# Optimization experiments

Measured on AMD Instinct MI355X. Metric: run time of the kernel, lower is better.

## Reference

```python
import jax, jax.numpy as jnp
import numpy as np

C, H = 256, 8
D = C // H
L, T, R = 2, 2, 3
OUT = 64
N = (30000, 50000)          # (author, paper)
F_IN = (128, 256)
E = (300000, 300000, 400000)
ETYPES = ((0, 1, 0), (1, 0, 1), (1, 1, 2))  # (src_type, dst_type, rel_idx)
SCALE = 1.0 / float(np.sqrt(D))


def setup_inputs() -> dict:
    key = jax.random.key(0)
    ks = iter(jax.random.split(key, 40))
    def nrm(shape, scale):
        return jax.random.normal(next(ks), shape, dtype=jnp.float32) * scale
    inp = {
        "x_author": nrm((N[0], F_IN[0]), 1.0),
        "x_paper": nrm((N[1], F_IN[1]), 1.0),
        "lin_in_author_W": nrm((F_IN[0], C), F_IN[0] ** -0.5),
        "lin_in_author_b": jnp.zeros((C,), jnp.float32),
        "lin_in_paper_W": nrm((F_IN[1], C), F_IN[1] ** -0.5),
        "lin_in_paper_b": jnp.zeros((C,), jnp.float32),
        "k_W": nrm((L, T, C, C), C ** -0.5), "k_b": jnp.zeros((L, T, C), jnp.float32),
        "q_W": nrm((L, T, C, C), C ** -0.5), "q_b": jnp.zeros((L, T, C), jnp.float32),
        "v_W": nrm((L, T, C, C), C ** -0.5), "v_b": jnp.zeros((L, T, C), jnp.float32),
        "a_W": nrm((L, R, H, D, D), D ** -0.5),
        "m_W": nrm((L, R, H, D, D), D ** -0.5),
        "p_rel": jnp.ones((L, R, H), jnp.float32),
        "skip": jnp.ones((L, T), jnp.float32),
        "out_W": nrm((L, T, C, C), C ** -0.5), "out_b": jnp.zeros((L, T, C), jnp.float32),
        "lin_out_W": nrm((C, OUT), C ** -0.5), "lin_out_b": jnp.zeros((OUT,), jnp.float32),
    }
    names = ("ei_writes", "ei_rev_writes", "ei_cites")
    for name, (s, d, _), e in zip(names, ETYPES, E):
        src = jax.random.randint(next(ks), (e,), 0, N[s], dtype=jnp.int32)
        dst = jax.random.randint(next(ks), (e,), 0, N[d], dtype=jnp.int32)
        inp[name] = jnp.stack([src, dst])
    inp["targetnode"] = 0
    return inp


def _seg_softmax(logits, seg, num_segments):
    # numerically stable softmax over ragged groups of edges sharing a dst node
    m = jax.ops.segment_max(logits, seg, num_segments=num_segments)
    m = jnp.where(jnp.isfinite(m), m, 0.0)
    ex = jnp.exp(logits - m[seg])
    s = jax.ops.segment_sum(ex, seg, num_segments=num_segments)
    return ex / (s[seg] + 1e-16)


def _hgt_forward(x_author, x_paper,
                 lin_in_author_W, lin_in_author_b, lin_in_paper_W, lin_in_paper_b,
                 k_W, k_b, q_W, q_b, v_W, v_b, a_W, m_W, p_rel, skip,
                 out_W, out_b, lin_out_W, lin_out_b, eis):
    # per-type input projection + relu
    xs = [
        jax.nn.relu(x_author @ lin_in_author_W + lin_in_author_b),
        jax.nn.relu(x_paper @ lin_in_paper_W + lin_in_paper_b),
    ]
    for l in range(L):
        # per node type k/q/v: [N_t, H, D]
        k = [(xs[t] @ k_W[l, t] + k_b[l, t]).reshape(N[t], H, D) for t in range(T)]
        q = [(xs[t] @ q_W[l, t] + q_b[l, t]).reshape(N[t], H, D) for t in range(T)]
        v = [(xs[t] @ v_W[l, t] + v_b[l, t]).reshape(N[t], H, D) for t in range(T)]
        agg = [jnp.zeros((N[t], H, D), xs[t].dtype) for t in range(T)]
        for (s, d, r), ei in zip(ETYPES, eis):
            src, dst = ei[0], ei[1]
            # relation-specific head-wise transforms of source keys/values
            k_r = jnp.einsum('nhd,hde->nhe', k[s], a_W[l, r])
            v_r = jnp.einsum('nhd,hde->nhe', v[s], m_W[l, r])
            # per-edge attention logits [E, H]
            alpha = jnp.einsum('ehd,ehd->eh', q[d][dst], k_r[src]) * p_rel[l, r] * SCALE
            w = _seg_softmax(alpha, dst, N[d])
            agg[d] = agg[d] + jax.ops.segment_sum(v_r[src] * w[..., None], dst,
                                                  num_segments=N[d])
        new_xs = []
        for t in range(T):
            o = jax.nn.gelu(agg[t].reshape(N[t], C)) @ out_W[l, t] + out_b[l, t]
            beta = jax.nn.sigmoid(skip[l, t])
            new_xs.append(beta * o + (1.0 - beta) * xs[t])
        xs = new_xs
    # shared output linear per node type
    return tuple(x @ lin_out_W + lin_out_b for x in xs)


def reference(x_author, x_paper, lin_in_author_W, lin_in_author_b,
              lin_in_paper_W, lin_in_paper_b, k_W, k_b, q_W, q_b, v_W, v_b,
              a_W, m_W, p_rel, skip, out_W, out_b, lin_out_W, lin_out_b,
              ei_writes, ei_rev_writes, ei_cites, targetnode):
    eis = (ei_writes, ei_rev_writes, ei_cites)
    return _hgt_forward(x_author, x_paper,
                        lin_in_author_W, lin_in_author_b,
                        lin_in_paper_W, lin_in_paper_b,
                        k_W, k_b, q_W, q_b, v_W, v_b, a_W, m_W, p_rel, skip,
                        out_W, out_b, lin_out_W, lin_out_b, eis)
```

## Files before the change

### kernel.cpp

```cpp
#include <hip/hip_runtime.h>


#define CC 256
#define HH 8
#define DD 32
#define LL 2
#define TT 2
#define RR 3
#define OUTD 64

typedef unsigned short bf16_t;
struct us4 { unsigned short x, y, z, w; };
typedef __attribute__((ext_vector_type(8))) short short8;
typedef __attribute__((ext_vector_type(4))) float f32x4;

__device__ __forceinline__ float b2f(unsigned short u) {
  return __uint_as_float(((unsigned)u) << 16);
}
__device__ __forceinline__ float blo(unsigned u) {
  return __uint_as_float(u << 16);
}
__device__ __forceinline__ float bhi(unsigned u) {
  return __uint_as_float(u & 0xFFFF0000u);
}
__device__ __forceinline__ unsigned short f2b(float f) {
  unsigned u = __float_as_uint(f);
  unsigned r = (u + 0x7FFFu + ((u >> 16) & 1u)) >> 16;
  return (unsigned short)r;
}
__device__ __forceinline__ float ld_dyn(const void* p, size_t e, bool isb) {
  return isb ? b2f(((const bf16_t*)p)[e]) : ((const float*)p)[e];
}
__device__ __forceinline__ float4 load4_dyn(const void* p, size_t e, bool isb) {
  if (isb) {
    us4 v = *(const us4*)((const bf16_t*)p + e);
    return make_float4(b2f(v.x), b2f(v.y), b2f(v.z), b2f(v.w));
  }
  return *(const float4*)((const float*)p + e);
}
__device__ __forceinline__ void st_dyn(void* p, size_t e, float v, bool isb) {
  if (isb) ((bf16_t*)p)[e] = f2b(v);
  else ((float*)p)[e] = v;
}
__device__ __forceinline__ float gelu1(float v) {
  const float t = tanhf(0.7978845608028654f * (v + 0.044715f * v * v * v));
  return 0.5f * v * (1.f + t);
}

__global__ void detect_kernel(const unsigned* __restrict__ probe,
                              int* __restrict__ flag) {
  *flag = (*probe == 0x3F800000u) ? 0 : 1;
}

__global__ __launch_bounds__(256) void prep_kernel(
    const void* __restrict__ xA, const void* __restrict__ xP,
    const void* __restrict__ WinA, const void* __restrict__ WinP,
    const void* __restrict__ qW, const void* __restrict__ outW,
    const void* __restrict__ binA, const void* __restrict__ binP,
    const void* __restrict__ qb, const void* __restrict__ ob,
    bf16_t* __restrict__ dq0, bf16_t* __restrict__ dq1,
    bf16_t* __restrict__ dWinAt, bf16_t* __restrict__ dWinPt,
    bf16_t* __restrict__ dqWt, bf16_t* __restrict__ doutWt,
    float* __restrict__ dbinA, float* __restrict__ dbinP,
    float* __restrict__ dqb, float* __restrict__ dob,
    int* __restrict__ zbase, int zn, int N0, int N1,
    const int* __restrict__ dflag) {
  const bool isb = (*dflag != 0);
  int gid = blockIdx.x * 256 + threadIdx.x;
  const int n0 = N0 * 128, n1 = N1 * 256;
  if (gid < n0) { dq0[gid] = f2b(ld_dyn(xA, gid, isb)); return; }
  gid -= n0;
  if (gid < n1) { dq1[gid] = f2b(ld_dyn(xP, gid, isb)); return; }
  gid -= n1;
  if (gid < 128 * 256) {
    const int n = gid % 256, k = gid / 256;
    dWinAt[n * 128 + k] = f2b(ld_dyn(WinA, gid, isb));
    return;
  }
  gid -= 128 * 256;
  if (gid < 256 * 256) {
    const int n = gid % 256, k = gid / 256;
    dWinPt[n * 256 + k] = f2b(ld_dyn(WinP, gid, isb));
    return;
  }
  gid -= 256 * 256;
  if (gid < 4 * 65536) {
    const int lt = gid >> 16, i = gid & 65535;
    const int n = i % 256, k = i / 256;
    dqWt[(size_t)lt * 65536 + n * 256 + k] =
        f2b(ld_dyn(qW, (size_t)lt * 65536 + i, isb));
    return;
  }
  gid -= 4 * 65536;
  if (gid < 4 * 65536) {
    const int lt = gid >> 16, i = gid & 65535;
    const int n = i % 256, k = i / 256;
    doutWt[(size_t)lt * 65536 + n * 256 + k] =
        f2b(ld_dyn(outW, (size_t)lt * 65536 + i, isb));
    return;
  }
  gid -= 4 * 65536;
  if (gid < 256) { dbinA[gid] = ld_dyn(binA, gid, isb); return; }
  gid -= 256;
  if (gid < 256) { dbinP[gid] = ld_dyn(binP, gid, isb); return; }
  gid -= 256;
  if (gid < 1024) { dqb[gid] = ld_dyn(qb, gid, isb); return; }
  gid -= 1024;
  if (gid < 1024) { dob[gid] = ld_dyn(ob, gid, isb); return; }
  gid -= 1024;
  if (gid < zn) zbase[gid] = 0;
}

__global__ __launch_bounds__(256) void fuse_w_kernel(
    const void* __restrict__ kW, const void* __restrict__ vW,
    const void* __restrict__ kb, const void* __restrict__ vb,
    const void* __restrict__ aW, const void* __restrict__ mW,
    bf16_t* __restrict__ Wcat, float* __restrict__ bcat,
    const int* __restrict__ dflag) {
  const bool isb = (*dflag != 0);
  const int lr = blockIdx.x;
  const int l = lr / RR;
  const int r = lr % RR;
  const int which = blockIdx.y;
  const int h = blockIdx.z;
  const int srct[RR] = {0, 1, 1};
  const int s = srct[r];
  __shared__ float Amat[DD][DD];
  const void* Ap = (which == 0 ? aW : mW);
  const size_t Apoff = (size_t)(lr * HH + h) * DD * DD;
  for (int i = threadIdx.x; i < DD * DD; i += 256)
    Amat[i / DD][i % DD] = ld_dyn(Ap, Apoff + i, isb);
  __syncthreads();
  const void* Wsrc = (which == 0 ? kW : vW);
  const void* bsrc = (which == 0 ? kb : vb);
  const size_t Wsoff = (size_t)(l * TT + s) * CC * CC;
  const size_t bsoff = (size_t)(l * TT + s) * CC;
  bf16_t* Wt = Wcat + (size_t)lr * 512 * CC;
  float* bdst = bcat + (size_t)lr * 512;
  const int c = threadIdx.x;
  float wrow[DD];
#pragma unroll
  for (int d = 0; d < DD; ++d)
    wrow[d] = ld_dyn(Wsrc, Wsoff + (size_t)c * CC + h * DD + d, isb);
#pragma unroll 4
  for (int e = 0; e < DD; ++e) {
    float acc = 0.f;
#pragma unroll
    for (int d = 0; d < DD; ++d) acc += wrow[d] * Amat[d][e];
    const int clo = h * DD + e;
    const int phys = ((clo >> 2) << 3) + (which << 2) + (clo & 3);
    Wt[(size_t)phys * CC + c] = f2b(acc);
  }
  if (c < DD) {
    float acc = 0.f;
#pragma unroll
    for (int d = 0; d < DD; ++d)
      acc += ld_dyn(bsrc, bsoff + h * DD + d, isb) * Amat[d][c];
    const int clo = h * DD + c;
    const int phys = ((clo >> 2) << 3) + (which << 2) + (clo & 3);
    bdst[phys] = acc;
  }
}

struct GSeg {
  const bf16_t* A;
  const bf16_t* Bt;
  const float* bias;
  const bf16_t* Sold;
  bf16_t* C;
  int M, N, K, epi, skipIdx, nbx, blk0;
};
struct GBatch {
  GSeg s[6];
  int nseg;
};

__global__ __launch_bounds__(256) void bgemm_kernel(
    GBatch gb, const void* __restrict__ skipv, const int* __restrict__ dflag) {
  __shared__ bf16_t Asb[128][72];
  __shared__ bf16_t Bsb[128][72];
  int si = 0;
#pragma unroll
  for (int t = 1; t < 6; ++t)
    if (t < gb.nseg && (int)blockIdx.x >= gb.s[t].blk0) si = t;
  const bf16_t* __restrict__ A = gb.s[si].A;
  const bf16_t* __restrict__ Bt = gb.s[si].Bt;
  const float* __restrict__ bias = gb.s[si].bias;
  const bf16_t* __restrict__ Sold = gb.s[si].Sold;
  bf16_t* __restrict__ Cm = gb.s[si].C;
  const int M = gb.s[si].M;
  const int N = gb.s[si].N;
  const int K = gb.s[si].K;
  const int epi = gb.s[si].epi;
  const int local = (int)blockIdx.x - gb.s[si].blk0;
  const int bn = (local % gb.s[si].nbx) * 128;
  const int bm = (local / gb.s[si].nbx) * 128;
  const int tid = threadIdx.x;
  const int wave = tid >> 6;
  const int lane = tid & 63;
  const int qd = lane >> 4;
  const int l16 = lane & 15;
  const int wm = (wave & 1) * 64;
  const int wn = (wave >> 1) * 64;
  f32x4 acc[4][4] = {};
  for (int k0 = 0; k0 < K; k0 += 64) {
#pragma unroll
    for (int i = 0; i < 4; ++i) {
      const int c = tid + 256 * i;
      const int row = c >> 3;
      const int col = (c & 7) * 8;
      uint4 va = make_uint4(0u, 0u, 0u, 0u);
      if (bm + row < M)
        va = *(const uint4*)(A + (size_t)(bm + row) * K + k0 + col);
      *(uint4*)&Asb[row][col] = va;
      const uint4 vb = *(const uint4*)(Bt + (size_t)(bn + row) * K + k0 + col);
      *(uint4*)&Bsb[row][col] = vb;
    }
    __syncthreads();
#pragma unroll
    for (int s = 0; s < 2; ++s) {
      short8 af[4], bf[4];
#pragma unroll
      for (int i = 0; i < 4; ++i) {
        af[i] = *(const short8*)&Asb[wm + i * 16 + l16][s * 32 + qd * 8];
        bf[i] = *(const short8*)&Bsb[wn + i * 16 + l16][s * 32 + qd * 8];
      }
#pragma unroll
      for (int mi = 0; mi < 4; ++mi)
#pragma unroll
        for (int ni = 0; ni < 4; ++ni)
          acc[mi][ni] = __builtin_amdgcn_mfma_f32_16x16x32_bf16(
              af[mi], bf[ni], acc[mi][ni], 0, 0, 0);
    }
    __syncthreads();
  }
  float beta = 0.f;
  if (epi == 2)
    beta = 1.f / (1.f + __expf(-ld_dyn(skipv, gb.s[si].skipIdx, *dflag != 0)));
#pragma unroll
  for (int mi = 0; mi < 4; ++mi) {
#pragma unroll
    for (int r = 0; r < 4; ++r) {
      const int row = bm + wm + mi * 16 + qd * 4 + r;
      if (row < M) {
#pragma unroll
        for (int ni = 0; ni < 4; ++ni) {
          const int col = bn + wn + ni * 16 + l16;
          float v = acc[mi][ni][r] + bias[col];
          if (epi == 1) v = fmaxf(v, 0.f);
          if (epi == 2)
            v = beta * v + (1.f - beta) * b2f(Sold[(size_t)row * N + col]);
          Cm[(size_t)row * N + col] = f2b(v);
        }
      }
    }
  }
}

__global__ __launch_bounds__(256) void fgemm2_kernel(
    const bf16_t* __restrict__ A0, int M0, const bf16_t* __restrict__ A1,
    int M1, const void* __restrict__ B, const void* __restrict__ bias,
    void* __restrict__ Cm, const int* __restrict__ dflag) {
  const bool isb = (*dflag != 0);
  __shared__ float As[32][68];
  __shared__ float Bs[32][64];
  const int nb0 = (M0 + 63) / 64;
  const bf16_t* A;
  int M, bm;
  size_t Coff;
  if ((int)blockIdx.x < nb0) {
    A = A0; M = M0; Coff = 0; bm = blockIdx.x * 64;
  } else {
    A = A1; M = M1; Coff = (size_t)M0 * OUTD; bm = (blockIdx.x - nb0) * 64;
  }
  const int tid = threadIdx.x;
  const int tx = tid & 15;
  const int ty = tid >> 4;
  float acc[4][4] = {};
  for (int k0 = 0; k0 < CC; k0 += 32) {
    {
      const int r = tid >> 3;
      const int c4 = (tid & 7) << 2;
#pragma unroll
      for (int rr = 0; rr < 2; ++rr) {
        const int row = bm + r + rr * 32;
        float4 v = make_float4(0.f, 0.f, 0.f, 0.f);
        if (row < M) v = load4_dyn(A, (size_t)row * CC + k0 + c4, true);
        As[c4 + 0][r + rr * 32] = v.x;
        As[c4 + 1][r + rr * 32] = v.y;
        As[c4 + 2][r + rr * 32] = v.z;
        As[c4 + 3][r + rr * 32] = v.w;
      }
    }
    {
      const int r = tid >> 4;
      const int c4 = (tid & 15) << 2;
#pragma unroll
      for (int rr = 0; rr < 2; ++rr) {
        const float4 v =
            load4_dyn(B, (size_t)(k0 + r + rr * 16) * OUTD + c4, isb);
        *(float4*)&Bs[r + rr * 16][c4] = v;
      }
    }
    __syncthreads();
#pragma unroll
    for (int kk = 0; kk < 32; ++kk) {
      const float4 av = *(const float4*)&As[kk][ty << 2];
      const float4 bv = *(const float4*)&Bs[kk][tx << 2];
      acc[0][0] += av.x * bv.x; acc[0][1] += av.x * bv.y;
      acc[0][2] += av.x * bv.z; acc[0][3] += av.x * bv.w;
      acc[1][0] += av.y * bv.x; acc[1][1] += av.y * bv.y;
      acc[1][2] += av.y * bv.z; acc[1][3] += av.y * bv.w;
      acc[2][0] += av.z * bv.x; acc[2][1] += av.z * bv.y;
      acc[2][2] += av.z * bv.z; acc[2][3] += av.z * bv.w;
      acc[3][0] += av.w * bv.x; acc[3][1] += av.w * bv.y;
      acc[3][2] += av.w * bv.z; acc[3][3] += av.w * bv.w;
    }
    __syncthreads();
  }
#pragma unroll
  for (int i = 0; i < 4; ++i) {
    const int row = bm + (ty << 2) + i;
    if (row < M) {
#pragma unroll
      for (int j = 0; j < 4; ++j) {
        const int col = (tx << 2) + j;
        const float v = acc[i][j] + ld_dyn(bias, col, isb);
        st_dyn(Cm, Coff + (size_t)row * OUTD + col, v, isb);
      }
    }
  }
}

__global__ void countA_kernel(const int* __restrict__ e0, int E0,
                              const int* __restrict__ e1, int E1,
                              const int* __restrict__ e2, int E2,
                              int* __restrict__ c0, int* __restrict__ c1,
                              int* __restrict__ c2) {
  int g = blockIdx.x * 256 + threadIdx.x;
  if (g < E0) { atomicAdd(&c0[e0[E0 + g]], 1); return; }
  g -= E0;
  if (g < E1) { atomicAdd(&c1[e1[E1 + g]], 1); return; }
  g -= E1;
  if (g < E2) atomicAdd(&c2[e2[E2 + g]], 1);
}

__global__ __launch_bounds__(256) void scan1A_kernel(
    const int* __restrict__ c0, int n0_, const int* __restrict__ c1, int n1_,
    const int* __restrict__ c2, int n2_, int* __restrict__ bsum, int nch0,
    int nch1) {
  int b = blockIdx.x;
  const int* c;
  int n, rel;
  if (b < nch0) { rel = 0; c = c0; n = n0_; }
  else if (b < nch0 + nch1) { rel = 1; c = c1; n = n1_; b -= nch0; }
  else { rel = 2; c = c2; n = n2_; b -= nch0 + nch1; }
  const int base = b * 1024;
  int s = 0;
#pragma unroll
  for (int j = 0; j < 4; ++j) {
    const int i = base + threadIdx.x + j * 256;
    s += (i < n) ? c[i] : 0;
  }
  __shared__ int red[256];
  red[threadIdx.x] = s;
  __syncthreads();
  for (int d = 128; d > 0; d >>= 1) {
    if (threadIdx.x < d) red[threadIdx.x] += red[threadIdx.x + d];
    __syncthreads();
  }
  if (threadIdx.x == 0) bsum[rel * 64 + b] = red[0];
}

__global__ __launch_bounds__(64) void scan2A_kernel(int* __restrict__ bsum,
                                                    int* __restrict__ totals,
                                                    int nch0, int nch1,
                                                    int nch2) {
  if (threadIdx.x != 0) return;
  const int rel = blockIdx.x;
  const int nch = (rel == 0) ? nch0 : (rel == 1) ? nch1 : nch2;
  int* bs = bsum + rel * 64;
  int run = 0;
  for (int i = 0; i < nch; ++i) {
    const int v = bs[i];
    bs[i] = run;
    run += v;
  }
  totals[rel] = run;
}

__global__ __launch_bounds__(256) void scan3A_kernel(
    const int* __restrict__ c0, int n0_, const int* __restrict__ c1, int n1_,
    const int* __restrict__ c2, int n2_, const int* __restrict__ bsum,
    const int* __restrict__ totals, int* __restrict__ ip0,
    int* __restrict__ ip1, int* __restrict__ ip2, int nch0, int nch1) {
  int b = blockIdx.x;
  const int* c;
  int* ip;
  int n, rel;
  if (b < nch0) { rel = 0; c = c0; n = n0_; ip = ip0; }
  else if (b < nch0 + nch1) { rel = 1; c = c1; n = n1_; ip = ip1; b -= nch0; }
  else { rel = 2; c = c2; n = n2_; ip = ip2; b -= nch0 + nch1; }
  const int base = b * 1024;
  int v[4];
  int s = 0;
#pragma unroll
  for (int j = 0; j < 4; ++j) {
    const int i = base + threadIdx.x * 4 + j;
    v[j] = (i < n) ? c[i] : 0;
    s += v[j];
  }
  __shared__ int ts[256];
  ts[threadIdx.x] = s;
  __syncthreads();
  for (int d = 1; d < 256; d <<= 1) {
    const int t = (threadIdx.x >= d) ? ts[threadIdx.x - d] : 0;
    __syncthreads();
    ts[threadIdx.x] += t;
    __syncthreads();
  }
  int run = bsum[rel * 64 + b] + ((threadIdx.x > 0) ? ts[threadIdx.x - 1] : 0);
#pragma unroll
  for (int j = 0; j < 4; ++j) {
    const int i = base + threadIdx.x * 4 + j;
    if (i < n) ip[i] = run;
    run += v[j];
  }
  if (b == 0 && threadIdx.x == 0) ip[n] = totals[rel];
}

__global__ void fillA_kernel(const int* __restrict__ e0, int E0,
                             const int* __restrict__ e1, int E1,
                             const int* __restrict__ e2, int E2,
                             const int* __restrict__ ip0,
                             const int* __restrict__ ip1,
                             const int* __restrict__ ip2, int* __restrict__ u0,
                             int* __restrict__ u1, int* __restrict__ u2,
                             int* __restrict__ s0, int* __restrict__ s1,
                             int* __restrict__ s2) {
  int g = blockIdx.x * 256 + threadIdx.x;
  const int* ei;
  const int* ip;
  int* cur;
  int* srcs;
  int E;
  if (g < E0) { ei = e0; E = E0; ip = ip0; cur = u0; srcs = s0; }
  else {
    g -= E0;
    if (g < E1) { ei = e1; E = E1; ip = ip1; cur = u1; srcs = s1; }
    else {
      g -= E1;
      if (g >= E2) return;
      ei = e2; E = E2; ip = ip2; cur = u2; srcs = s2;
    }
  }
  const int d = ei[E + g];
  const int pos = ip[d] + atomicAdd(&cur[d], 1);
  srcs[pos] = ei[g];
}

template <int NREL>
__global__ __launch_bounds__(256) void aggf3_kernel(
    const bf16_t* __restrict__ q, const uint4* __restrict__ kv0,
    const int* __restrict__ ip0, const int* __restrict__ ss0, int po0,
    const uint4* __restrict__ kv1, const int* __restrict__ ip1,
    const int* __restrict__ ss1, int po1, const void* __restrict__ prel,
    float scale, bf16_t* __restrict__ outb, int Nd,
    const int* __restrict__ dflag) {
  const bool isb = (*dflag != 0);
  const int d = blockIdx.x * 4 + (threadIdx.x >> 6);
  if (d >= Nd) return;
  const int lane = threadIdx.x & 63;
  const int hM = lane >> 3;
  const us4 qv = ((const us4*)q)[(size_t)d * 64 + lane];
  const float q0 = b2f(qv.x), q1 = b2f(qv.y), q2 = b2f(qv.z), q3 = b2f(qv.w);
  float a0 = 0.f, a1 = 0.f, a2 = 0.f, a3 = 0.f;

#define LDBLK(P, X0, X1, X2, X3)                       \
  {                                                    \
    const int pm_ = p1v - 1;                           \
    int i1_ = (P) + 1, i2_ = (P) + 2, i3_ = (P) + 3;   \
    i1_ = i1_ > pm_ ? pm_ : i1_;                       \
    i2_ = i2_ > pm_ ? pm_ : i2_;                       \
    i3_ = i3_ > pm_ ? pm_ : i3_;                       \
    X0 = kv[(size_t)ss[(P)] * 64 + lane];              \
    X1 = kv[(size_t)ss[i1_] * 64 + lane];              \
    X2 = kv[(size_t)ss[i2_] * 64 + lane];              \
    X3 = kv[(size_t)ss[i3_] * 64 + lane];              \
  }

#define CPTBLK(P, X0, X1, X2, X3)                                             \
  {                                                                           \
    float t0 = q0 * blo(X0.x) + q1 * bhi(X0.x) + q2 * blo(X0.y) + q3 * bhi(X0.y); \
    float t1 = q0 * blo(X1.x) + q1 * bhi(X1.x) + q2 * blo(X1.y) + q3 * bhi(X1.y); \
    float t2 = q0 * blo(X2.x) + q1 * bhi(X2.x) + q2 * blo(X2.y) + q3 * bhi(X2.y); \
    float t3 = q0 * blo(X3.x) + q1 * bhi(X3.x) + q2 * blo(X3.y) + q3 * bhi(X3.y); \
    t0 += __shfl_xor(t0, 1, 8); t1 += __shfl_xor(t1, 1, 8);                   \
    t2 += __shfl_xor(t2, 1, 8); t3 += __shfl_xor(t3, 1, 8);                   \
    t0 += __shfl_xor(t0, 2, 8); t1 += __shfl_xor(t1, 2, 8);                   \
    t2 += __shfl_xor(t2, 2, 8); t3 += __shfl_xor(t3, 2, 8);                   \
    t0 += __shfl_xor(t0, 4, 8); t1 += __shfl_xor(t1, 4, 8);                   \
    t2 += __shfl_xor(t2, 4, 8); t3 += __shfl_xor(t3, 4, 8);                   \
    float l0 = t0 * ph, l1 = t1 * ph, l2 = t2 * ph, l3 = t3 * ph;             \
    const int rem_ = p1v - (P);                                               \
    if (rem_ < 4) {                                                           \
      if (rem_ <= 1) l1 = -1.0e38f;                                           \
      if (rem_ <= 2) l2 = -1.0e38f;                                           \
      l3 = -1.0e38f;                                                          \
    }                                                                         \
    const float mn = fmaxf(fmaxf(fmaxf(l0, l1), fmaxf(l2, l3)), m);           \
    const float sc = __expf(m - mn);                                          \
    const float w0 = __expf(l0 - mn);                                         \
    const float w1 = __expf(l1 - mn);                                         \
    const float w2 = __expf(l2 - mn);                                         \
    const float w3 = __expf(l3 - mn);                                         \
    lsum = lsum * sc + (w0 + w1 + w2 + w3);                                   \
    b0 = b0 * sc + w0 * blo(X0.z) + w1 * blo(X1.z) + w2 * blo(X2.z) + w3 * blo(X3.z); \
    b1 = b1 * sc + w0 * bhi(X0.z) + w1 * bhi(X1.z) + w2 * bhi(X2.z) + w3 * bhi(X3.z); \
    b2 = b2 * sc + w0 * blo(X0.w) + w1 * blo(X1.w) + w2 * blo(X2.w) + w3 * blo(X3.w); \
    b3 = b3 * sc + w0 * bhi(X0.w) + w1 * bhi(X1.w) + w2 * bhi(X2.w) + w3 * bhi(X3.w); \
    m = mn;                                                                   \
  }

#pragma unroll
  for (int rel = 0; rel < NREL; ++rel) {
    const uint4* kv = rel ? kv1 : kv0;
    const int* ip = rel ? ip1 : ip0;
    const int* ss = rel ? ss1 : ss0;
    const float ph = ld_dyn(prel, (rel ? po1 : po0) + hM, isb) * scale;
    const int p0v = ip[d];
    const int p1v = ip[d + 1];
    if (p0v == p1v) continue;
    float m = -3.0e38f, lsum = 0.f;
    float b0 = 0.f, b1 = 0.f, b2 = 0.f, b3 = 0.f;
    uint4 A0, A1, A2, A3, B0, B1, B2, B3;
    int p = p0v;
    LDBLK(p, A0, A1, A2, A3);
    for (;;) {
      if (p + 4 < p1v) LDBLK(p + 4, B0, B1, B2, B3);
      CPTBLK(p, A0, A1, A2, A3);
      p += 4;
      if (p >= p1v) break;
      if (p + 4 < p1v) LDBLK(p + 4, A0, A1, A2, A3);
      CPTBLK(p, B0, B1, B2, B3);
      p += 4;
      if (p >= p1v) break;
    }
    const float inv = 1.f / (lsum + 1e-16f);
    a0 += b0 * inv;
    a1 += b1 * inv;
    a2 += b2 * inv;
    a3 += b3 * inv;
  }
#undef LDBLK
#undef CPTBLK
  us4 r;
  r.x = f2b(gelu1(a0));
  r.y = f2b(gelu1(a1));
  r.z = f2b(gelu1(a2));
  r.w = f2b(gelu1(a3));
  ((us4*)outb)[(size_t)d * 64 + lane] = r;
}

extern "C" void kernel_launch(void* const* d_in, const int* in_sizes, int n_in,
                              void* d_out, int out_size, void* d_ws,
                              size_t ws_size, hipStream_t stream) {
  const void* xA = d_in[0];
  const void* xP = d_in[1];
  const void* WinA = d_in[2];
  const void* binA = d_in[3];
  const void* WinP = d_in[4];
  const void* binP = d_in[5];
  const void* kW = d_in[6];
  const void* kb = d_in[7];
  const void* qW = d_in[8];
  const void* qb = d_in[9];
  const void* vW = d_in[10];
  const void* vb = d_in[11];
  const void* aW = d_in[12];
  const void* mW = d_in[13];
  const void* prel = d_in[14];
  const void* skipv = d_in[15];
  const void* outW = d_in[16];
  const void* outb = d_in[17];
  const void* WoutL = d_in[18];
  const void* boutL = d_in[19];
  const int* eiA[RR] = {(const int*)d_in[20], (const int*)d_in[21],
                        (const int*)d_in[22]};
  const int Ecnt[RR] = {in_sizes[20] / 2, in_sizes[21] / 2, in_sizes[22] / 2};
  const int N0 = in_sizes[0] / 128;
  const int N1 = in_sizes[1] / 256;
  const float SCALE = 0.17677669529663687f;
  (void)n_in; (void)out_size;

  float* w = (float*)d_ws;
  size_t off = 0;
  auto alloc = [&](size_t nf) { float* p = w + off; off += (nf + 3) & ~3ull; return p; };
  int* dflag = (int*)alloc(4);
  bf16_t* xsb[TT];
  xsb[0] = (bf16_t*)alloc((size_t)N0 * CC / 2);
  xsb[1] = (bf16_t*)alloc((size_t)N1 * CC / 2);
  bf16_t* qbuf[TT];
  qbuf[0] = (bf16_t*)alloc((size_t)N0 * CC / 2);
  qbuf[1] = (bf16_t*)alloc((size_t)N1 * CC / 2);
  bf16_t* buf_a = (bf16_t*)alloc((size_t)N0 * 512 / 2);
  bf16_t* buf_p = (bf16_t*)alloc((size_t)N1 * 512 / 2);
  bf16_t* Wcat = (bf16_t*)alloc((size_t)LL * RR * 512 * CC / 2);
  float* bcat = alloc((size_t)LL * RR * 512);
  bf16_t* qWt = (bf16_t*)alloc((size_t)LL * TT * CC * CC / 2);
  bf16_t* outWt = (bf16_t*)alloc((size_t)LL * TT * CC * CC / 2);
  bf16_t* WinAt = (bf16_t*)alloc((size_t)CC * 128 / 2);
  bf16_t* WinPt = (bf16_t*)alloc((size_t)CC * CC / 2);
  float* binAf = alloc(CC);
  float* binPf = alloc(CC);
  float* qbf = alloc((size_t)LL * TT * CC);
  float* outbf = alloc((size_t)LL * TT * CC);
  int* indptr[RR];
  int* srcs[RR];
  for (int r = 0; r < RR; ++r) {
    const int nd = (r == 1) ? N0 : N1;
    indptr[r] = (int*)alloc((size_t)nd + 1);
    srcs[r] = (int*)alloc((size_t)Ecnt[r]);
  }
  const int zn = 2 * (2 * N1 + N0);
  int* cntall = (int*)alloc((size_t)zn);
  int* cnt0 = cntall;           int* cur0 = cnt0 + N1;
  int* cnt1 = cur0 + N1;        int* cur1 = cnt1 + N0;
  int* cnt2 = cur1 + N0;        int* cur2 = cnt2 + N1;
  int* bsum = (int*)alloc(3 * 64);
  int* stotal = (int*)alloc(4);
  bf16_t* buf_p2 = (bf16_t*)alloc((size_t)N1 * 512 / 2);
  const bool haveP2 = (off * 4) <= ws_size;
  if (!haveP2) buf_p2 = buf_p;

  detect_kernel<<<1, 1, 0, stream>>>((const unsigned*)skipv, dflag);

  {
    const size_t total = (size_t)N0 * 128 + (size_t)N1 * 256 + 128 * 256 +
                         256 * 256 + 4 * 65536 + 4 * 65536 + 256 + 256 + 1024 +
                         1024 + zn;
    prep_kernel<<<(int)((total + 255) / 256), 256, 0, stream>>>(
        xA, xP, WinA, WinP, qW, outW, binA, binP, qb, outb, qbuf[0], qbuf[1],
        WinAt, WinPt, qWt, outWt, binAf, binPf, qbf, outbf, cntall, zn, N0, N1,
        dflag);
  }
  fuse_w_kernel<<<dim3(LL * RR, 2, HH), 256, 0, stream>>>(
      kW, vW, kb, vb, aW, mW, Wcat, bcat, dflag);

  {
    const int E0 = Ecnt[0], E1 = Ecnt[1], E2 = Ecnt[2];
    const int nch0 = (N1 + 1023) / 1024;
    const int nch1 = (N0 + 1023) / 1024;
    const int nch2 = (N1 + 1023) / 1024;
    const int EG = (E0 + E1 + E2 + 255) / 256;
    countA_kernel<<<EG, 256, 0, stream>>>(eiA[0], E0, eiA[1], E1, eiA[2], E2,
                                          cnt0, cnt1, cnt2);
    scan1A_kernel<<<nch0 + nch1 + nch2, 256, 0, stream>>>(
        cnt0, N1, cnt1, N0, cnt2, N1, bsum, nch0, nch1);
    scan2A_kernel<<<3, 64, 0, stream>>>(bsum, stotal, nch0, nch1, nch2);
    scan3A_kernel<<<nch0 + nch1 + nch2, 256, 0, stream>>>(
        cnt0, N1, cnt1, N0, cnt2, N1, bsum, stotal, indptr[0], indptr[1],
        indptr[2], nch0, nch1);
    fillA_kernel<<<EG, 256, 0, stream>>>(eiA[0], E0, eiA[1], E1, eiA[2], E2,
                                         indptr[0], indptr[1], indptr[2], cur0,
                                         cur1, cur2, srcs[0], srcs[1], srcs[2]);
  }

  auto launch_batch = [&](GBatch& gb) {
    int tot = 0;
    for (int i = 0; i < gb.nseg; ++i) {
      gb.s[i].nbx = gb.s[i].N / 128;
      gb.s[i].blk0 = tot;
      tot += gb.s[i].nbx * ((gb.s[i].M + 127) / 128);
    }
    bgemm_kernel<<<tot, 256, 0, stream>>>(gb, skipv, dflag);
  };
  auto seg = [](const bf16_t* A, const bf16_t* Bt, const float* bias,
                const bf16_t* Sold, bf16_t* C, int M, int N, int K, int epi,
                int skipIdx) {
    GSeg s;
    s.A = A; s.Bt = Bt; s.bias = bias; s.Sold = Sold; s.C = C;
    s.M = M; s.N = N; s.K = K; s.epi = epi; s.skipIdx = skipIdx;
    s.nbx = 0; s.blk0 = 0;
    return s;
  };

  {
    GBatch b{};
    b.s[0] = seg(qbuf[1], WinPt, binPf, nullptr, xsb[1], N1, CC, 256, 1, 0);
    b.s[1] = seg(qbuf[0], WinAt, binAf, nullptr, xsb[0], N0, CC, 128, 1, 0);
    b.nseg = 2;
    launch_batch(b);
  }

  for (int l = 0; l < LL; ++l) {
    const int lt0 = l * TT + 0, lt1 = l * TT + 1;
    const int lr0 = l * RR + 0, lr1 = l * RR + 1, lr2 = l * RR + 2;
    {
      GBatch b{};
      int n = 0;
      b.s[n++] = seg(xsb[1], Wcat + (size_t)lr1 * 512 * CC,
                     bcat + (size_t)lr1 * 512, nullptr, buf_p, N1, 512, CC, 0, 0);
      if (haveP2)
        b.s[n++] = seg(xsb[1], Wcat + (size_t)lr2 * 512 * CC,
                       bcat + (size_t)lr2 * 512, nullptr, buf_p2, N1, 512, CC,
                       0, 0);
      b.s[n++] = seg(xsb[0], Wcat + (size_t)lr0 * 512 * CC,
                     bcat + (size_t)lr0 * 512, nullptr, buf_a, N0, 512, CC, 0, 0);
      b.s[n++] = seg(xsb[1], qWt + (size_t)lt1 * CC * CC,
                     qbf + (size_t)lt1 * CC, nullptr, qbuf[1], N1, CC, CC, 0, 0);
      b.s[n++] = seg(xsb[0], qWt + (size_t)lt0 * CC * CC,
                     qbf + (size_t)lt0 * CC, nullptr, qbuf[0], N0, CC, CC, 0, 0);
      b.nseg = n;
      launch_batch(b);
    }
    aggf3_kernel<1><<<(N0 + 3) / 4, 256, 0, stream>>>(
        qbuf[0], (const uint4*)buf_p, indptr[1], srcs[1], lr1 * HH, nullptr,
        nullptr, nullptr, 0, prel, SCALE, qbuf[0], N0, dflag);
    if (!haveP2) {
      GBatch b{};
      b.s[0] = seg(xsb[1], Wcat + (size_t)lr2 * 512 * CC,
                   bcat + (size_t)lr2 * 512, nullptr, buf_p, N1, 512, CC, 0, 0);
      b.nseg = 1;
      launch_batch(b);
    }
    aggf3_kernel<2><<<(N1 + 3) / 4, 256, 0, stream>>>(
        qbuf[1], (const uint4*)buf_a, indptr[0], srcs[0], lr0 * HH,
        (const uint4*)buf_p2, indptr[2], srcs[2], lr2 * HH, prel, SCALE,
        qbuf[1], N1, dflag);
    {
      GBatch b{};
      b.s[0] = seg(qbuf[1], outWt + (size_t)lt1 * CC * CC,
                   outbf + (size_t)lt1 * CC, xsb[1], xsb[1], N1, CC, CC, 2, lt1);
      b.s[1] = seg(qbuf[0], outWt + (size_t)lt0 * CC * CC,
                   outbf + (size_t)lt0 * CC, xsb[0], xsb[0], N0, CC, CC, 2, lt0);
      b.nseg = 2;
      launch_batch(b);
    }
  }

  fgemm2_kernel<<<(N0 + 63) / 64 + (N1 + 63) / 64, 256, 0, stream>>>(
      xsb[0], N0, xsb[1], N1, WoutL, boutL, d_out, dflag);
}
```

Measured before the change: 1.187 ms.

## Merge per-type aggregation launches and remap GEMM block order across XCDs

```diff
diff --git a/kernel.cpp b/kernel.cpp
--- a/kernel.cpp
+++ b/kernel.cpp
@@ -173,16 +173,24 @@
 struct GBatch {
   GSeg s[6];
   int nseg;
+  int tot;
 };
 
 __global__ __launch_bounds__(256) void bgemm_kernel(
     GBatch gb, const void* __restrict__ skipv, const int* __restrict__ dflag) {
   __shared__ bf16_t Asb[128][72];
   __shared__ bf16_t Bsb[128][72];
+  int bid;
+  {
+    const int h = (int)blockIdx.x;
+    const int q8 = gb.tot >> 3, r8 = gb.tot & 7;
+    const int x = h & 7, idx = h >> 3;
+    bid = x * q8 + (x < r8 ? x : r8) + idx;
+  }
   int si = 0;
 #pragma unroll
   for (int t = 1; t < 6; ++t)
-    if (t < gb.nseg && (int)blockIdx.x >= gb.s[t].blk0) si = t;
+    if (t < gb.nseg && bid >= gb.s[t].blk0) si = t;
   const bf16_t* __restrict__ A = gb.s[si].A;
   const bf16_t* __restrict__ Bt = gb.s[si].Bt;
   const float* __restrict__ bias = gb.s[si].bias;
@@ -192,7 +200,7 @@
   const int N = gb.s[si].N;
   const int K = gb.s[si].K;
   const int epi = gb.s[si].epi;
-  const int local = (int)blockIdx.x - gb.s[si].blk0;
+  const int local = bid - gb.s[si].blk0;
   const int bn = (local % gb.s[si].nbx) * 128;
   const int bm = (local / gb.s[si].nbx) * 128;
   const int tid = threadIdx.x;
@@ -460,15 +468,15 @@
 }
 
 template <int NREL>
-__global__ __launch_bounds__(256) void aggf3_kernel(
-    const bf16_t* __restrict__ q, const uint4* __restrict__ kv0,
+__device__ __forceinline__ void aggf_body(
+    int blk, const bf16_t* __restrict__ q, const uint4* __restrict__ kv0,
     const int* __restrict__ ip0, const int* __restrict__ ss0, int po0,
     const uint4* __restrict__ kv1, const int* __restrict__ ip1,
     const int* __restrict__ ss1, int po1, const void* __restrict__ prel,
     float scale, bf16_t* __restrict__ outb, int Nd,
     const int* __restrict__ dflag) {
   const bool isb = (*dflag != 0);
-  const int d = blockIdx.x * 4 + (threadIdx.x >> 6);
+  const int d = blk * 4 + (threadIdx.x >> 6);
   if (d >= Nd) return;
   const int lane = threadIdx.x & 63;
   const int hM = lane >> 3;
@@ -562,6 +570,37 @@
   ((us4*)outb)[(size_t)d * 64 + lane] = r;
 }
 
+template <int NREL>
+__global__ __launch_bounds__(256) void aggf3_kernel(
+    const bf16_t* __restrict__ q, const uint4* __restrict__ kv0,
+    const int* __restrict__ ip0, const int* __restrict__ ss0, int po0,
+    const uint4* __restrict__ kv1, const int* __restrict__ ip1,
+    const int* __restrict__ ss1, int po1, const void* __restrict__ prel,
+    float scale, bf16_t* __restrict__ outb, int Nd,
+    const int* __restrict__ dflag) {
+  aggf_body<NREL>(blockIdx.x, q, kv0, ip0, ss0, po0, kv1, ip1, ss1, po1, prel,
+                  scale, outb, Nd, dflag);
+}
+
+__global__ __launch_bounds__(256) void aggm_kernel(
+    const bf16_t* __restrict__ qP, const uint4* __restrict__ kvP0,
+    const int* __restrict__ ipP0, const int* __restrict__ ssP0, int poP0,
+    const uint4* __restrict__ kvP1, const int* __restrict__ ipP1,
+    const int* __restrict__ ssP1, int poP1, bf16_t* __restrict__ outP,
+    int NdP, int nblkP, const bf16_t* __restrict__ qA,
+    const uint4* __restrict__ kvA, const int* __restrict__ ipA,
+    const int* __restrict__ ssA, int poA, bf16_t* __restrict__ outA, int NdA,
+    const void* __restrict__ prel, float scale,
+    const int* __restrict__ dflag) {
+  if ((int)blockIdx.x < nblkP) {
+    aggf_body<2>(blockIdx.x, qP, kvP0, ipP0, ssP0, poP0, kvP1, ipP1, ssP1,
+                 poP1, prel, scale, outP, NdP, dflag);
+  } else {
+    aggf_body<1>((int)blockIdx.x - nblkP, qA, kvA, ipA, ssA, poA, nullptr,
+                 nullptr, nullptr, 0, prel, scale, outA, NdA, dflag);
+  }
+}
+
 extern "C" void kernel_launch(void* const* d_in, const int* in_sizes, int n_in,
                               void* d_out, int out_size, void* d_ws,
                               size_t ws_size, hipStream_t stream) {
@@ -673,6 +712,7 @@
       gb.s[i].blk0 = tot;
       tot += gb.s[i].nbx * ((gb.s[i].M + 127) / 128);
     }
+    gb.tot = tot;
     bgemm_kernel<<<tot, 256, 0, stream>>>(gb, skipv, dflag);
   };
   auto seg = [](const bf16_t* A, const bf16_t* Bt, const float* bias,
@@ -714,20 +754,28 @@
       b.nseg = n;
       launch_batch(b);
     }
-    aggf3_kernel<1><<<(N0 + 3) / 4, 256, 0, stream>>>(
-        qbuf[0], (const uint4*)buf_p, indptr[1], srcs[1], lr1 * HH, nullptr,
-        nullptr, nullptr, 0, prel, SCALE, qbuf[0], N0, dflag);
-    if (!haveP2) {
+    if (haveP2) {
+      const int nblkP = (N1 + 3) / 4;
+      const int nblkA = (N0 + 3) / 4;
+      aggm_kernel<<<nblkP + nblkA, 256, 0, stream>>>(
+          qbuf[1], (const uint4*)buf_a, indptr[0], srcs[0], lr0 * HH,
+          (const uint4*)buf_p2, indptr[2], srcs[2], lr2 * HH, qbuf[1], N1,
+          nblkP, qbuf[0], (const uint4*)buf_p, indptr[1], srcs[1], lr1 * HH,
+          qbuf[0], N0, prel, SCALE, dflag);
+    } else {
+      aggf3_kernel<1><<<(N0 + 3) / 4, 256, 0, stream>>>(
+          qbuf[0], (const uint4*)buf_p, indptr[1], srcs[1], lr1 * HH, nullptr,
+          nullptr, nullptr, 0, prel, SCALE, qbuf[0], N0, dflag);
       GBatch b{};
       b.s[0] = seg(xsb[1], Wcat + (size_t)lr2 * 512 * CC,
                    bcat + (size_t)lr2 * 512, nullptr, buf_p, N1, 512, CC, 0, 0);
       b.nseg = 1;
       launch_batch(b);
-    }
-    aggf3_kernel<2><<<(N1 + 3) / 4, 256, 0, stream>>>(
-        qbuf[1], (const uint4*)buf_a, indptr[0], srcs[0], lr0 * HH,
-        (const uint4*)buf_p2, indptr[2], srcs[2], lr2 * HH, prel, SCALE,
-        qbuf[1], N1, dflag);
+      aggf3_kernel<2><<<(N1 + 3) / 4, 256, 0, stream>>>(
+          qbuf[1], (const uint4*)buf_a, indptr[0], srcs[0], lr0 * HH,
+          (const uint4*)buf_p, indptr[2], srcs[2], lr2 * HH, prel, SCALE,
+          qbuf[1], N1, dflag);
+    }
     {
       GBatch b{};
       b.s[0] = seg(qbuf[1], outWt + (size_t)lt1 * CC * CC,
```

After: 1.112 ms. -6.4%, faster.
